# Performance work log

Hardware: AMD Instinct MI355X
Metric: run time of the kernel (lower is better)

## Reference

```python
import jax, jax.numpy as jnp
import numpy as np

B, H, W, D, HEADS, WS, SHIFT = 64, 28, 28, 384, 12, 7, 3
N = WS * WS  # tokens per window = 49
HEAD_DIM = D // HEADS
SCALE = HEAD_DIM ** -0.5


def _rel_pos_index():
    # standard Swin relative position index, shape [N, N], values in [0, (2*WS-1)^2)
    coords = np.stack(np.meshgrid(np.arange(WS), np.arange(WS), indexing='ij'))  # [2,ws,ws]
    cf = coords.reshape(2, -1)  # [2, N]
    rel = (cf[:, :, None] - cf[:, None, :]).transpose(1, 2, 0).astype(np.int64)  # [N,N,2]
    rel[:, :, 0] += WS - 1
    rel[:, :, 1] += WS - 1
    rel[:, :, 0] *= 2 * WS - 1
    return rel.sum(-1)  # [N, N]


def _attn_mask():
    # shifted-window mask, shape [nW, N, N], entries 0 or -100
    img = np.zeros((H, W))
    cnt = 0
    sl = (slice(0, -WS), slice(-WS, -SHIFT), slice(-SHIFT, None))
    for hs in sl:
        for ws_ in sl:
            img[hs, ws_] = cnt
            cnt += 1
    mw = img.reshape(H // WS, WS, W // WS, WS).transpose(0, 2, 1, 3).reshape(-1, N)  # [nW, N]
    diff = mw[:, None, :] - mw[:, :, None]  # unsqueeze(1) - unsqueeze(2)
    return np.where(diff != 0, -100.0, 0.0).astype(np.float32)


_REL_IDX = _rel_pos_index()
_ATTN_MASK = _attn_mask()


def _ln(x, g, b, eps=1e-5):
    m = x.mean(-1, keepdims=True)
    v = ((x - m) ** 2).mean(-1, keepdims=True)
    return (x - m) * jax.lax.rsqrt(v + eps) * g + b


def _window_partition(x):
    # [B,H,W,C] -> [B*nW, N, C]
    Bz, _, _, C = x.shape
    x = x.reshape(Bz, H // WS, WS, W // WS, WS, C).transpose(0, 1, 3, 2, 4, 5)
    return x.reshape(-1, N, C)


def _window_reverse(xw, Bz):
    # [B*nW, N, C] -> [B,H,W,C]
    C = xw.shape[-1]
    x = xw.reshape(Bz, H // WS, W // WS, WS, WS, C).transpose(0, 1, 3, 2, 4, 5)
    return x.reshape(Bz, H, W, C)


def setup_inputs() -> dict:
    key = jax.random.key(0)
    ks = jax.random.split(key, 12)
    s = 0.02
    return {
        'x': jax.random.normal(ks[0], (B, H * W, D), jnp.float32),
        'norm1_g': jnp.ones((D,), jnp.float32),
        'norm1_b': jnp.zeros((D,), jnp.float32),
        'qkv_w': jax.random.normal(ks[1], (D, 3 * D), jnp.float32) * s,
        'qkv_b': jnp.zeros((3 * D,), jnp.float32),
        'proj_w': jax.random.normal(ks[2], (D, D), jnp.float32) * s,
        'proj_b': jnp.zeros((D,), jnp.float32),
        'rpb_table': jax.random.normal(ks[3], ((2 * WS - 1) ** 2, HEADS), jnp.float32) * s,
        'norm2_g': jnp.ones((D,), jnp.float32),
        'norm2_b': jnp.zeros((D,), jnp.float32),
        'fc1_w': jax.random.normal(ks[4], (D, 4 * D), jnp.float32) * s,
        'fc1_b': jnp.zeros((4 * D,), jnp.float32),
        'fc2_w': jax.random.normal(ks[5], (4 * D, D), jnp.float32) * s,
        'fc2_b': jnp.zeros((D,), jnp.float32),
    }


def reference(x, norm1_g, norm1_b, qkv_w, qkv_b, proj_w, proj_b, rpb_table,
              norm2_g, norm2_b, fc1_w, fc1_b, fc2_w, fc2_b):
    Bz = x.shape[0]
    nW = (H // WS) * (W // WS)
    shortcut = x
    h = _ln(x, norm1_g, norm1_b).reshape(Bz, H, W, D)
    # cyclic shift
    h = jnp.roll(h, shift=(-SHIFT, -SHIFT), axis=(1, 2))
    xw = _window_partition(h)  # [B*nW, N, D]
    # windowed attention
    qkv = (xw @ qkv_w + qkv_b).reshape(-1, N, 3, HEADS, HEAD_DIM)
    q, k, v = [qkv[:, :, i].transpose(0, 2, 1, 3) for i in range(3)]  # [B*nW, H, N, hd]
    attn = jnp.einsum('whnd,whmd->whnm', q * SCALE, k)
    bias = rpb_table[jnp.asarray(_REL_IDX)]  # [N,N,HEADS]
    attn = attn + bias.transpose(2, 0, 1)[None]
    mask = jnp.asarray(_ATTN_MASK)  # [nW,N,N]
    attn = attn.reshape(Bz, nW, HEADS, N, N) + mask[None, :, None]
    attn = jax.nn.softmax(attn.reshape(-1, HEADS, N, N), axis=-1)
    out = jnp.einsum('whnm,whmd->whnd', attn, v)  # [B*nW, H, N, hd]
    out = out.transpose(0, 2, 1, 3).reshape(-1, N, D)
    out = out @ proj_w + proj_b
    # reverse windows + reverse shift
    h = _window_reverse(out, Bz)
    h = jnp.roll(h, shift=(SHIFT, SHIFT), axis=(1, 2)).reshape(Bz, H * W, D)
    x = shortcut + h
    # MLP
    m = _ln(x, norm2_g, norm2_b)
    m = jax.nn.gelu(m @ fc1_w + fc1_b, approximate=False)
    m = m @ fc2_w + fc2_b
    return x + m
```

## Files before the change

### kernel.cpp

```cpp
#include <hip/hip_runtime.h>

typedef unsigned short u16;
typedef unsigned int u32;
typedef __bf16 bf16x8 __attribute__((ext_vector_type(8)));
typedef float f32x4 __attribute__((ext_vector_type(4)));
typedef u32 u32x4 __attribute__((ext_vector_type(4)));
typedef u32 u32x2 __attribute__((ext_vector_type(2)));

union U8 { u32x4 u; u16 us[8]; bf16x8 bf; };

static __device__ __forceinline__ float b2f(u16 h) {
  union { u32 i; float f; } c; c.i = ((u32)h) << 16; return c.f;
}
static __device__ __forceinline__ u16 f2b(float f) {
  union { float f; u32 i; } c; c.f = f;
  u32 x = c.i;
  return (u16)((x + 0x7fffu + ((x >> 16) & 1u)) >> 16);
}

#define G2LDS16(gp, lp)                                                                   \
  __builtin_amdgcn_global_load_lds((const __attribute__((address_space(1))) void*)(gp),   \
                                   (__attribute__((address_space(3))) void*)(lp), 16, 0, 0)

__global__ __launch_bounds__(256) void wtrans(const float* __restrict__ W, u16* __restrict__ WT,
                                              int K, int N) {
  __shared__ float t[32][33];
  int n0 = blockIdx.x * 32, k0 = blockIdx.y * 32;
  int tx = threadIdx.x, ty = threadIdx.y;
#pragma unroll
  for (int r = 0; r < 4; ++r)
    t[ty + 8 * r][tx] = W[(long)(k0 + ty + 8 * r) * N + n0 + tx];
  __syncthreads();
#pragma unroll
  for (int r = 0; r < 4; ++r)
    WT[(long)(n0 + ty + 8 * r) * K + k0 + tx] = f2b(t[tx][ty + 8 * r]);
}

template<int MODE>
__global__ __launch_bounds__(256) void ln_kernel(const float* __restrict__ src,
                                                 const float* __restrict__ g,
                                                 const float* __restrict__ b,
                                                 u16* __restrict__ dst) {
  int tok = blockIdx.x * 4 + (threadIdx.x >> 6);
  int lane = threadIdx.x & 63;
  long srow;
  if (MODE == 0) {
    int wg = tok / 49, i = tok % 49;
    int bimg = wg >> 4, wloc = wg & 15;
    int wh = wloc >> 2, ww = wloc & 3;
    int ih = i / 7, iw = i % 7;
    int hr = wh * 7 + ih + 3; if (hr >= 28) hr -= 28;
    int wr = ww * 7 + iw + 3; if (wr >= 28) wr -= 28;
    srow = (long)(bimg * 784 + hr * 28 + wr) * 384;
  } else {
    srow = (long)tok * 384;
  }
  const float* p = src + srow + lane * 6;
  float v[6];
#pragma unroll
  for (int t = 0; t < 6; ++t) v[t] = p[t];
  float s = 0.f, ss = 0.f;
#pragma unroll
  for (int t = 0; t < 6; ++t) { s += v[t]; ss += v[t] * v[t]; }
  for (int m = 32; m; m >>= 1) { s += __shfl_xor(s, m); ss += __shfl_xor(ss, m); }
  float mean = s * (1.0f / 384.0f);
  float var  = ss * (1.0f / 384.0f) - mean * mean;
  float rs = rsqrtf(var + 1e-5f);
  u16* o = dst + (long)tok * 384 + lane * 6;
#pragma unroll
  for (int t = 0; t < 6; ++t)
    o[t] = f2b((v[t] - mean) * rs * g[lane * 6 + t] + b[lane * 6 + t]);
}

template<int EPI>
__global__ __launch_bounds__(256, 2) void gemm_big(
    const u16* __restrict__ A, const u16* __restrict__ BT,
    const float* __restrict__ bias, const float* __restrict__ xres,
    u16* __restrict__ Cb, float* __restrict__ Cf, int N, int K) {
  __shared__ __align__(16) u16 As0[128 * 64];
  __shared__ __align__(16) u16 As1[128 * 64];
  __shared__ __align__(16) u16 Bs0[128 * 64];
  __shared__ __align__(16) u16 Bs1[128 * 64];
  const int tid = threadIdx.x;
  const int wave = tid >> 6, lane = tid & 63, quad = lane >> 4, col = lane & 15;

  const int NY = (EPI == 0) ? 9 : (EPI == 1) ? 12 : 3;
  const int nwg = gridDim.x * gridDim.y;
  const int id = blockIdx.x + blockIdx.y * gridDim.x;
  const int sid = (id & 7) * (nwg >> 3) + (id >> 3);
  const int mi = sid / NY, ni = sid - mi * NY;
  const long m0 = (long)mi * 128;
  const int n0 = ni * 128;

  const int rm = (wave & 1) * 64, cn = (wave >> 1) * 64;
  f32x4 acc[4][4];
#pragma unroll
  for (int i = 0; i < 4; ++i)
#pragma unroll
    for (int j = 0; j < 4; ++j) acc[i][j] = f32x4{0.f, 0.f, 0.f, 0.f};

  const int K64 = K >> 6;
  const int sr = lane >> 3;
  const int sc = (lane & 7) ^ sr;
  const u16* gA = A  + (m0 + wave * 32 + sr) * (long)K + sc * 8;
  const u16* gB = BT + ((long)(n0 + wave * 32 + sr)) * K + sc * 8;

#define STAGE(kt, AS, BS)                                                        \
  {                                                                              \
    _Pragma("unroll")                                                            \
    for (int c = 0; c < 4; ++c) {                                                \
      G2LDS16(gA + (long)c * 8 * K + (kt) * 64, &AS[wave * 2048 + c * 512]);     \
      G2LDS16(gB + (long)c * 8 * K + (kt) * 64, &BS[wave * 2048 + c * 512]);     \
    }                                                                            \
  }

#define COMPUTE(AS, BS)                                                          \
  {                                                                              \
    _Pragma("unroll")                                                            \
    for (int kk = 0; kk < 2; ++kk) {                                             \
      U8 af[4], bfr[4];                                                          \
      _Pragma("unroll")                                                          \
      for (int i = 0; i < 4; ++i) {                                              \
        int row = rm + i * 16 + col;                                             \
        int slot = (kk * 4 + quad) ^ (row & 7);                                  \
        af[i].u = *(const u32x4*)&AS[row * 64 + slot * 8];                       \
      }                                                                          \
      _Pragma("unroll")                                                          \
      for (int j = 0; j < 4; ++j) {                                              \
        int row = cn + j * 16 + col;                                             \
        int slot = (kk * 4 + quad) ^ (row & 7);                                  \
        bfr[j].u = *(const u32x4*)&BS[row * 64 + slot * 8];                      \
      }                                                                          \
      _Pragma("unroll")                                                          \
      for (int i = 0; i < 4; ++i)                                                \
        _Pragma("unroll")                                                        \
        for (int j = 0; j < 4; ++j)                                              \
          acc[i][j] = __builtin_amdgcn_mfma_f32_16x16x32_bf16(af[i].bf, bfr[j].bf, acc[i][j], 0, 0, 0); \
    }                                                                            \
  }

  STAGE(0, As0, Bs0);
  __syncthreads();
  for (int kt = 0; kt < K64; kt += 2) {
    if (kt + 1 < K64) STAGE(kt + 1, As1, Bs1);
    COMPUTE(As0, Bs0);
    __syncthreads();
    if (kt + 2 < K64) STAGE(kt + 2, As0, Bs0);
    COMPUTE(As1, Bs1);
    __syncthreads();
  }
#undef STAGE
#undef COMPUTE

#pragma unroll
  for (int j = 0; j < 4; ++j) {
    int n = n0 + cn + j * 16 + col;
    float bv = bias[n];
#pragma unroll
    for (int i = 0; i < 4; ++i) {
#pragma unroll
      for (int rr = 0; rr < 4; ++rr) {
        int row = (int)m0 + rm + i * 16 + quad * 4 + rr;
        float v = acc[i][j][rr] + bv;
        if (EPI == 0) {
          Cb[(long)row * N + n] = f2b(v);
        } else if (EPI == 1) {
          float gl = 0.5f * v * (1.0f + erff(v * 0.70710678118654752f));
          Cb[(long)row * N + n] = f2b(gl);
        } else if (EPI == 2) {
          int wg = row / 49, i49 = row - wg * 49;
          int bimg = wg >> 4, wloc = wg & 15;
          int wh = wloc >> 2, ww = wloc & 3;
          int ih = i49 / 7, iw = i49 - (i49 / 7) * 7;
          int ho = wh * 7 + ih + 3; if (ho >= 28) ho -= 28;
          int wo = ww * 7 + iw + 3; if (wo >= 28) wo -= 28;
          long dst = (long)(bimg * 784 + ho * 28 + wo) * 384 + n;
          Cf[dst] = v + xres[dst];
        } else {
          long idx = (long)row * 384 + n;
          Cf[idx] = v + Cf[idx];
        }
      }
    }
  }
}

__global__ __launch_bounds__(256) void bmt_kernel(const float* __restrict__ rpb,
                                                  float* __restrict__ bmt) {
  int th = blockIdx.y;
  int type = th / 12, head = th - type * 12;
  int e = blockIdx.x * 256 + threadIdx.x;
  int tj = e >> 8, ti = (e >> 6) & 3, quad = (e >> 4) & 3, c = e & 15;
  int i = ti * 16 + c;
  int ih = i / 7, iw = i - ih * 7;
  int regi = ((type & 2) ? ((ih < 4) ? 1 : 2) : 0) * 3 + ((type & 1) ? ((iw < 4) ? 1 : 2) : 0);
  f32x4 v;
#pragma unroll
  for (int r = 0; r < 4; ++r) {
    int j = tj * 16 + quad * 4 + r;
    float val = -1e30f;
    if (i < 49 && j < 49) {
      int jh = j / 7, jw = j - jh * 7;
      int idx = (ih - jh + 6) * 13 + (iw - jw + 6);
      val = rpb[idx * 12 + head];
      int regj = ((type & 2) ? ((jh < 4) ? 1 : 2) : 0) * 3 + ((type & 1) ? ((jw < 4) ? 1 : 2) : 0);
      if (regi != regj) val -= 100.0f;
    }
    v[r] = val;
  }
  ((f32x4*)bmt)[((long)th * 16 + tj * 4 + ti) * 64 + quad * 16 + c] = v;
}

__global__ __launch_bounds__(256) void attn_kernel(const u16* __restrict__ qkv,
                                                   const float* __restrict__ bmt,
                                                   u16* __restrict__ obuf) {
  __shared__ __align__(16) u16 Ks[64 * 136];
  __shared__ __align__(16) u16 Vs[64 * 130];
  __shared__ __align__(16) u16 PL[4 * 64 * 72];
  const int w = blockIdx.x, h0 = blockIdx.y * 4;
  const int tid = threadIdx.x;
  const int hl = tid >> 6, lane = tid & 63, quad = lane >> 4, c = lane & 15;
  const int head = h0 + hl;
  const int wloc = w & 15;
  const int type = (((wloc >> 2) == 3) ? 2 : 0) + (((wloc & 3) == 3) ? 1 : 0);

#pragma unroll
  for (int it = 0; it < 4; ++it) {
    int cc = tid + it * 256;
    int j = cc >> 4, ch = cc & 15;
    u32x4 val = {0u, 0u, 0u, 0u};
    if (j < 49)
      val = *(const u32x4*)(qkv + ((long)w * 49 + j) * 1152 + 384 + h0 * 32 + ch * 8);
    *(u32x4*)&Ks[j * 136 + ch * 8] = val;
  }
#pragma unroll
  for (int it = 0; it < 16; ++it) {
    int cc = tid + it * 256;
    int j = cc >> 6, c4 = cc & 63;
    u32 val = 0u;
    if (j < 49)
      val = *(const u32*)(qkv + ((long)w * 49 + j) * 1152 + 768 + h0 * 32 + c4 * 2);
    *(u32*)&Vs[j * 130 + c4 * 2] = val;
  }

  U8 qf[4];
#pragma unroll
  for (int ti = 0; ti < 4; ++ti)
    qf[ti].u = *(const u32x4*)(qkv + ((long)w * 49 + ti * 16 + c) * 1152 + head * 32 + quad * 8);
  __syncthreads();

  U8 kf[4];
#pragma unroll
  for (int tj = 0; tj < 4; ++tj)
    kf[tj].u = *(const u32x4*)&Ks[(tj * 16 + c) * 136 + hl * 32 + quad * 8];
  f32x4 s[4][4];
#pragma unroll
  for (int tj = 0; tj < 4; ++tj)
#pragma unroll
    for (int ti = 0; ti < 4; ++ti)
      s[tj][ti] = __builtin_amdgcn_mfma_f32_16x16x32_bf16(kf[tj].bf, qf[ti].bf,
                                                          f32x4{0.f, 0.f, 0.f, 0.f}, 0, 0, 0);

  const f32x4* btb = (const f32x4*)bmt + ((long)(type * 12 + head) * 16) * 64 + quad * 16 + c;
#pragma unroll
  for (int tj = 0; tj < 4; ++tj)
#pragma unroll
    for (int ti = 0; ti < 4; ++ti) {
      f32x4 bv = btb[(tj * 4 + ti) * 64];
#pragma unroll
      for (int r = 0; r < 4; ++r)
        s[tj][ti][r] = fmaf(s[tj][ti][r], 0.17677669529663689f, bv[r]);
    }

#pragma unroll
  for (int ti = 0; ti < 4; ++ti) {
    float m = -1e30f;
#pragma unroll
    for (int tj = 0; tj < 4; ++tj)
#pragma unroll
      for (int r = 0; r < 4; ++r) m = fmaxf(m, s[tj][ti][r]);
    m = fmaxf(m, __shfl_xor(m, 16));
    m = fmaxf(m, __shfl_xor(m, 32));
    float l = 0.f;
#pragma unroll
    for (int tj = 0; tj < 4; ++tj)
#pragma unroll
      for (int r = 0; r < 4; ++r) {
        float p = __expf(s[tj][ti][r] - m);
        s[tj][ti][r] = p;
        l += p;
      }
    l += __shfl_xor(l, 16);
    l += __shfl_xor(l, 32);
    float inv = 1.0f / l;
#pragma unroll
    for (int tj = 0; tj < 4; ++tj)
#pragma unroll
      for (int r = 0; r < 4; ++r) s[tj][ti][r] *= inv;
  }

#pragma unroll
  for (int ti = 0; ti < 4; ++ti)
#pragma unroll
    for (int tj = 0; tj < 4; ++tj) {
      u32 lo = (u32)f2b(s[tj][ti][0]) | ((u32)f2b(s[tj][ti][1]) << 16);
      u32 hi = (u32)f2b(s[tj][ti][2]) | ((u32)f2b(s[tj][ti][3]) << 16);
      *(u32x2*)&PL[hl * 4608 + (ti * 16 + c) * 72 + tj * 16 + quad * 4] = u32x2{lo, hi};
    }

  f32x4 oacc[4][2];
#pragma unroll
  for (int t2 = 0; t2 < 4; ++t2) {
    oacc[t2][0] = f32x4{0.f, 0.f, 0.f, 0.f};
    oacc[t2][1] = f32x4{0.f, 0.f, 0.f, 0.f};
  }
#pragma unroll
  for (int kk = 0; kk < 2; ++kk) {
    U8 pa[4];
#pragma unroll
    for (int t2 = 0; t2 < 4; ++t2)
      pa[t2].u = *(const u32x4*)&PL[hl * 4608 + (t2 * 16 + c) * 72 + kk * 32 + quad * 8];
    U8 vf[2];
#pragma unroll
    for (int td = 0; td < 2; ++td)
#pragma unroll
      for (int e = 0; e < 8; ++e)
        vf[td].us[e] = Vs[(kk * 32 + quad * 8 + e) * 130 + hl * 32 + td * 16 + c];
#pragma unroll
    for (int t2 = 0; t2 < 4; ++t2)
#pragma unroll
      for (int td = 0; td < 2; ++td)
        oacc[t2][td] = __builtin_amdgcn_mfma_f32_16x16x32_bf16(pa[t2].bf, vf[td].bf, oacc[t2][td], 0, 0, 0);
  }

#pragma unroll
  for (int t2 = 0; t2 < 4; ++t2)
#pragma unroll
    for (int r = 0; r < 4; ++r) {
      int i = t2 * 16 + quad * 4 + r;
      if (i < 49) {
        u16* op = obuf + ((long)w * 49 + i) * 384 + head * 32 + c;
        op[0]  = f2b(oacc[t2][0][r]);
        op[16] = f2b(oacc[t2][1][r]);
      }
    }
}

extern "C" void kernel_launch(void* const* d_in, const int* in_sizes, int n_in,
                              void* d_out, int out_size, void* d_ws, size_t ws_size,
                              hipStream_t stream) {
  const float* x     = (const float*)d_in[0];
  const float* n1g   = (const float*)d_in[1];
  const float* n1b   = (const float*)d_in[2];
  const float* qkvw  = (const float*)d_in[3];
  const float* qkvb  = (const float*)d_in[4];
  const float* projw = (const float*)d_in[5];
  const float* projb = (const float*)d_in[6];
  const float* rpb   = (const float*)d_in[7];
  const float* n2g   = (const float*)d_in[8];
  const float* n2b   = (const float*)d_in[9];
  const float* fc1w  = (const float*)d_in[10];
  const float* fc1b  = (const float*)d_in[11];
  const float* fc2w  = (const float*)d_in[12];
  const float* fc2b  = (const float*)d_in[13];
  float* out = (float*)d_out;

  u16* qkvwT  = (u16*)d_ws;
  u16* projwT = qkvwT + 442368;
  u16* fc1wT  = projwT + 147456;
  u16* fc2wT  = fc1wT + 589824;
  u16* wsA    = fc2wT + 589824;
  u16* wsB    = wsA + 19267584;
  u16* xw   = wsA;
  u16* obuf = wsA;
  u16* abuf = wsA;
  u16* qkvB = wsB;
  u16* midB = wsB;
  float* bmtb = (float*)qkvwT;

  wtrans<<<dim3(36, 12), dim3(32, 8), 0, stream>>>(qkvw, qkvwT, 384, 1152);
  wtrans<<<dim3(12, 12), dim3(32, 8), 0, stream>>>(projw, projwT, 384, 384);
  wtrans<<<dim3(48, 12), dim3(32, 8), 0, stream>>>(fc1w, fc1wT, 384, 1536);
  wtrans<<<dim3(12, 48), dim3(32, 8), 0, stream>>>(fc2w, fc2wT, 1536, 384);

  ln_kernel<0><<<12544, 256, 0, stream>>>(x, n1g, n1b, xw);
  gemm_big<0><<<dim3(392, 9), 256, 0, stream>>>(xw, qkvwT, qkvb, nullptr, qkvB, nullptr, 1152, 384);
  bmt_kernel<<<dim3(4, 48), 256, 0, stream>>>(rpb, bmtb);
  attn_kernel<<<dim3(1024, 3), 256, 0, stream>>>(qkvB, bmtb, obuf);
  gemm_big<2><<<dim3(392, 3), 256, 0, stream>>>(obuf, projwT, projb, x, nullptr, out, 384, 384);
  ln_kernel<1><<<12544, 256, 0, stream>>>(out, n2g, n2b, abuf);
  gemm_big<1><<<dim3(392, 12), 256, 0, stream>>>(abuf, fc1wT, fc1b, nullptr, midB, nullptr, 1536, 384);
  gemm_big<3><<<dim3(392, 3), 256, 0, stream>>>(midB, fc2wT, fc2b, nullptr, nullptr, out, 384, 1536);
}
```

Before: 562.5 us.

## Vectorize epilogues via transposed MFMA, tanh GELU, packed bf16 conversion

The GEMM swaps the MFMA operand order so each lane holds four consecutive output columns. Every epilogue can then use vector bias, residual and output loads and stores, where before it wrote scalar values with row-strided access. The exact erf GELU is replaced by a tanh-style sigmoid approximation, and the software bf16 rounding is replaced by the hardware packed convert instruction. LayerNorm loads and stores are also vectorized with float2 and packed bf16. The GELU approximation changes numerics slightly.

Measured after the change: 572.3 us. Within noise of the previous version (+1.7%).

```diff
diff --git a/kernel.cpp b/kernel.cpp
--- a/kernel.cpp
+++ b/kernel.cpp
@@ -16,6 +16,17 @@
   union { float f; u32 i; } c; c.f = f;
   u32 x = c.i;
   return (u16)((x + 0x7fffu + ((x >> 16) & 1u)) >> 16);
+}
+static __device__ __forceinline__ u32 pk2(float a, float b) {
+  u32 d;
+  asm("v_cvt_pk_bf16_f32 %0, %1, %2" : "=v"(d) : "v"(a), "v"(b));
+  return d;
+}
+static __device__ __forceinline__ float gelu_f(float v) {
+  float v2 = v * v;
+  float ny2 = -2.0f * v * fmaf(0.0356774081f, v2, 0.7978845608f);
+  float sig = __builtin_amdgcn_rcpf(1.0f + __expf(ny2));
+  return v * sig;
 }
 
 #define G2LDS16(gp, lp)                                                                   \
@@ -55,10 +66,13 @@
   } else {
     srow = (long)tok * 384;
   }
-  const float* p = src + srow + lane * 6;
+  const float* p = src + srow;
   float v[6];
 #pragma unroll
-  for (int t = 0; t < 6; ++t) v[t] = p[t];
+  for (int t = 0; t < 3; ++t) {
+    float2 z = *(const float2*)(p + (lane + 64 * t) * 2);
+    v[2 * t] = z.x; v[2 * t + 1] = z.y;
+  }
   float s = 0.f, ss = 0.f;
 #pragma unroll
   for (int t = 0; t < 6; ++t) { s += v[t]; ss += v[t] * v[t]; }
@@ -66,10 +80,16 @@
   float mean = s * (1.0f / 384.0f);
   float var  = ss * (1.0f / 384.0f) - mean * mean;
   float rs = rsqrtf(var + 1e-5f);
-  u16* o = dst + (long)tok * 384 + lane * 6;
-#pragma unroll
-  for (int t = 0; t < 6; ++t)
-    o[t] = f2b((v[t] - mean) * rs * g[lane * 6 + t] + b[lane * 6 + t]);
+  u16* o = dst + (long)tok * 384;
+#pragma unroll
+  for (int t = 0; t < 3; ++t) {
+    int ch = (lane + 64 * t) * 2;
+    float2 gg = *(const float2*)(g + ch);
+    float2 bb = *(const float2*)(b + ch);
+    float r0 = (v[2 * t] - mean) * rs * gg.x + bb.x;
+    float r1 = (v[2 * t + 1] - mean) * rs * gg.y + bb.y;
+    *(u32*)&o[ch] = pk2(r0, r1);
+  }
 }
 
 template<int EPI>
@@ -95,9 +115,9 @@
   const int rm = (wave & 1) * 64, cn = (wave >> 1) * 64;
   f32x4 acc[4][4];
 #pragma unroll
-  for (int i = 0; i < 4; ++i)
-#pragma unroll
-    for (int j = 0; j < 4; ++j) acc[i][j] = f32x4{0.f, 0.f, 0.f, 0.f};
+  for (int j = 0; j < 4; ++j)
+#pragma unroll
+    for (int i = 0; i < 4; ++i) acc[j][i] = f32x4{0.f, 0.f, 0.f, 0.f};
 
   const int K64 = K >> 6;
   const int sr = lane >> 3;
@@ -132,10 +152,10 @@
         bfr[j].u = *(const u32x4*)&BS[row * 64 + slot * 8];                      \
       }                                                                          \
       _Pragma("unroll")                                                          \
-      for (int i = 0; i < 4; ++i)                                                \
+      for (int j = 0; j < 4; ++j)                                                \
         _Pragma("unroll")                                                        \
-        for (int j = 0; j < 4; ++j)                                              \
-          acc[i][j] = __builtin_amdgcn_mfma_f32_16x16x32_bf16(af[i].bf, bfr[j].bf, acc[i][j], 0, 0, 0); \
+        for (int i = 0; i < 4; ++i)                                              \
+          acc[j][i] = __builtin_amdgcn_mfma_f32_16x16x32_bf16(bfr[j].bf, af[i].bf, acc[j][i], 0, 0, 0); \
     }                                                                            \
   }
 
@@ -152,34 +172,53 @@
 #undef STAGE
 #undef COMPUTE
 
-#pragma unroll
-  for (int j = 0; j < 4; ++j) {
-    int n = n0 + cn + j * 16 + col;
-    float bv = bias[n];
+  if (EPI == 0 || EPI == 1) {
+#pragma unroll
+    for (int j = 0; j < 4; ++j) {
+      int nb = n0 + cn + j * 16 + quad * 4;
+      f32x4 bv = *(const f32x4*)&bias[nb];
+#pragma unroll
+      for (int i = 0; i < 4; ++i) {
+        long row = m0 + rm + i * 16 + col;
+        f32x4 v = acc[j][i] + bv;
+        if (EPI == 1) {
+#pragma unroll
+          for (int r = 0; r < 4; ++r) v[r] = gelu_f(v[r]);
+        }
+        *(u32x2*)&Cb[row * N + nb] = u32x2{pk2(v[0], v[1]), pk2(v[2], v[3])};
+      }
+    }
+  } else if (EPI == 2) {
 #pragma unroll
     for (int i = 0; i < 4; ++i) {
-#pragma unroll
-      for (int rr = 0; rr < 4; ++rr) {
-        int row = (int)m0 + rm + i * 16 + quad * 4 + rr;
-        float v = acc[i][j][rr] + bv;
-        if (EPI == 0) {
-          Cb[(long)row * N + n] = f2b(v);
-        } else if (EPI == 1) {
-          float gl = 0.5f * v * (1.0f + erff(v * 0.70710678118654752f));
-          Cb[(long)row * N + n] = f2b(gl);
-        } else if (EPI == 2) {
-          int wg = row / 49, i49 = row - wg * 49;
-          int bimg = wg >> 4, wloc = wg & 15;
-          int wh = wloc >> 2, ww = wloc & 3;
-          int ih = i49 / 7, iw = i49 - (i49 / 7) * 7;
-          int ho = wh * 7 + ih + 3; if (ho >= 28) ho -= 28;
-          int wo = ww * 7 + iw + 3; if (wo >= 28) wo -= 28;
-          long dst = (long)(bimg * 784 + ho * 28 + wo) * 384 + n;
-          Cf[dst] = v + xres[dst];
-        } else {
-          long idx = (long)row * 384 + n;
-          Cf[idx] = v + Cf[idx];
-        }
+      int row = (int)m0 + rm + i * 16 + col;
+      int wg = row / 49, i49 = row - wg * 49;
+      int bimg = wg >> 4, wloc = wg & 15;
+      int wh = wloc >> 2, ww = wloc & 3;
+      int ih = i49 / 7, iw = i49 - (i49 / 7) * 7;
+      int ho = wh * 7 + ih + 3; if (ho >= 28) ho -= 28;
+      int wo = ww * 7 + iw + 3; if (wo >= 28) wo -= 28;
+      long dstb = (long)(bimg * 784 + ho * 28 + wo) * 384;
+#pragma unroll
+      for (int j = 0; j < 4; ++j) {
+        int nb = n0 + cn + j * 16 + quad * 4;
+        f32x4 bv = *(const f32x4*)&bias[nb];
+        f32x4 xr = *(const f32x4*)&xres[dstb + nb];
+        f32x4 v = acc[j][i] + bv + xr;
+        *(f32x4*)&Cf[dstb + nb] = v;
+      }
+    }
+  } else {
+#pragma unroll
+    for (int i = 0; i < 4; ++i) {
+      long rb = (long)((int)m0 + rm + i * 16 + col) * 384;
+#pragma unroll
+      for (int j = 0; j < 4; ++j) {
+        int nb = n0 + cn + j * 16 + quad * 4;
+        f32x4 bv = *(const f32x4*)&bias[nb];
+        f32x4 old = *(const f32x4*)&Cf[rb + nb];
+        f32x4 v = acc[j][i] + bv + old;
+        *(f32x4*)&Cf[rb + nb] = v;
       }
     }
   }
@@ -303,8 +342,8 @@
   for (int ti = 0; ti < 4; ++ti)
 #pragma unroll
     for (int tj = 0; tj < 4; ++tj) {
-      u32 lo = (u32)f2b(s[tj][ti][0]) | ((u32)f2b(s[tj][ti][1]) << 16);
-      u32 hi = (u32)f2b(s[tj][ti][2]) | ((u32)f2b(s[tj][ti][3]) << 16);
+      u32 lo = pk2(s[tj][ti][0], s[tj][ti][1]);
+      u32 hi = pk2(s[tj][ti][2], s[tj][ti][3]);
       *(u32x2*)&PL[hl * 4608 + (ti * 16 + c) * 72 + tj * 16 + quad * 4] = u32x2{lo, hi};
     }
 
```
